# Performance work log

Hardware: AMD Instinct MI355X
Metric: run time of the kernel (lower is better)

## Reference

```python
import jax, jax.numpy as jnp
import numpy as np


def setup_inputs() -> dict:
    key = jax.random.key(0)
    k1, k2, k3 = jax.random.split(key, 3)
    preds = jax.random.normal(k1, (8, 3, 2048, 8), dtype=jnp.float32)
    gts = jax.random.normal(k2, (8, 3, 2048), dtype=jnp.float32)
    idx = jax.random.randint(k3, (64, 2), 0, 8, dtype=jnp.int64)
    return {"preds": preds, "gts": gts, "idx": idx}


def reference(preds, gts, idx):
    # preds: [bs, 3, N, seeds], gts: [bs, 3, N], idx: [num, 2] (batch, seed)
    num = idx.shape[0]
    # select (batch, seed) pairs -> [num, 3, N]
    p = jnp.transpose(preds, (0, 3, 1, 2))[idx[:, 0], idx[:, 1]]
    # gts expanded over seeds is constant in seed -> just index batch
    g = gts[idx[:, 0]]  # [num, 3, N]
    x = jnp.transpose(p, (0, 2, 1))  # [num, N, 3]
    y = jnp.transpose(g, (0, 2, 1))  # [num, N, 3]
    # P[b, i, j] = ||x_i||^2 + ||y_j||^2 - 2 x_i . y_j
    rx = jnp.sum(x * x, axis=-1)  # [num, N]
    ry = jnp.sum(y * y, axis=-1)  # [num, N]
    zz = jnp.einsum('bid,bjd->bij', x, y)  # [num, N, N]
    P = rx[:, :, None] + ry[:, None, :] - 2.0 * zz
    loss_1 = jnp.sum(jnp.min(P, axis=1))  # min over x for each y
    loss_2 = jnp.sum(jnp.min(P, axis=2))  # min over y for each x
    return (loss_1 + loss_2) / num
```

## Files before the change

kernel.cpp:

```cpp
#include <hip/hip_runtime.h>


#define NPTS 2048
#define NB 64
#define BLK 256

#define PREDS_A 49152
#define PREDS_C 16384
#define GTS_A 6144
#define GTS_C 2048

#define OFF_ROW   0
#define OFF_COL   524288
#define OFF_PART  1048576
#define OFF_YPK   1052672
#define WS_REQ    (OFF_YPK + NB * NPTS * 32)

using bf16x8  = __attribute__((ext_vector_type(8))) __bf16;
using short8v = __attribute__((ext_vector_type(8))) short;
using f32x16  = __attribute__((ext_vector_type(16))) float;

static __device__ __forceinline__ unsigned short f2bf(float f) {
    unsigned u = __float_as_uint(f);
    u = u + 0x7FFFu + ((u >> 16) & 1u);
    return (unsigned short)(u >> 16);
}
static __device__ __forceinline__ float bf2f(unsigned short h) {
    return __uint_as_float(((unsigned)h) << 16);
}
static __device__ __forceinline__ float min3f(float a, float b, float c) {
    return fminf(fminf(a, b), c);
}
static __device__ __forceinline__ float ctree(f32x16 a) {
    const float c0 = min3f(a[0], a[1], a[2]);
    const float c1 = min3f(a[3], a[4], a[5]);
    const float c2 = min3f(a[6], a[7], a[8]);
    const float c3 = min3f(a[9], a[10], a[11]);
    const float c4 = min3f(a[12], a[13], a[14]);
    const float d0 = min3f(c0, c1, a[15]);
    const float d1 = min3f(c2, c3, c4);
    return fminf(d0, d1);
}

__global__ __launch_bounds__(256) void cf_prep(
    const float* __restrict__ gts, const int* __restrict__ idx,
    unsigned* __restrict__ colbuf, unsigned short* __restrict__ ypk)
{
    const int blk = blockIdx.x, tid = threadIdx.x;
    if (blk < 512) {
        colbuf[blk * 256 + tid] = 0x7F800000u;
    } else {
        const unsigned short one = 0x3F80;
        const int p = (blk - 512) * 256 + tid;
        const int b = p >> 11, j = p & 2047;
        const int i0 = idx[2 * b];
        const float* gb = gts + i0 * GTS_A + j;
        const float y0 = gb[0], y1 = gb[GTS_C], y2 = gb[2 * GTS_C];
        const float ry = fmaf(y0, y0, fmaf(y1, y1, y2 * y2));
        const unsigned short h0 = f2bf(y0), h1 = f2bf(y1), h2 = f2bf(y2);
        const unsigned short l0 = f2bf(y0 - bf2f(h0));
        const unsigned short l1 = f2bf(y1 - bf2f(h1));
        const unsigned short l2 = f2bf(y2 - bf2f(h2));
        const unsigned short rh = f2bf(ry), rl = f2bf(ry - bf2f(rh));
        alignas(16) unsigned short t[16] =
            {h0, h1, h2, l0, l1, l2, h0, h1, h2, one, one, rh, rl, 0, 0, 0};
        uint4* dst = (uint4*)(ypk + (size_t)p * 16);
        dst[0] = *(const uint4*)&t[0];
        dst[1] = *(const uint4*)&t[8];
    }
}

__global__ __launch_bounds__(BLK, 4) void cf_mf4(
    const float* __restrict__ preds, const int* __restrict__ idx,
    const unsigned short* __restrict__ ypk,
    float* __restrict__ rowbuf, unsigned* __restrict__ colbuf)
{
    const int tid = threadIdx.x;
    const int strip = blockIdx.x & 15;
    const int b = blockIdx.x >> 4;

    __shared__ float scolw[4][NPTS];

    const int l = tid & 63, w = tid >> 6;
    const int lc = l & 31, lh = l >> 5;

    const int i0 = idx[2 * b], m1 = idx[2 * b + 1];
    {
    }
    const float* pb = preds + i0 * PREDS_A + m1 + (strip * 128 + w * 32 + lc) * 8;
    const float x0 = pb[0], x1 = pb[PREDS_C], x2 = pb[2 * PREDS_C];
    const float rx = fmaf(x0, x0, fmaf(x1, x1, x2 * x2));
    const float a0 = -2.f * x0, a1 = -2.f * x1, a2 = -2.f * x2;
    const unsigned short h0 = f2bf(a0), h1 = f2bf(a1), h2 = f2bf(a2);
    const unsigned short lo0 = f2bf(a0 - bf2f(h0));
    const unsigned short lo1 = f2bf(a1 - bf2f(h1));
    const unsigned short lo2 = f2bf(a2 - bf2f(h2));
    const unsigned short rh = f2bf(rx), rl = f2bf(rx - bf2f(rh));
    const unsigned short one = 0x3F80;
    short8v av;
    av[0] = (short)(lh ? lo2 : h0);
    av[1] = (short)(lh ? rh  : h1);
    av[2] = (short)(lh ? rl  : h2);
    av[3] = (short)(lh ? one : h0);
    av[4] = (short)(lh ? one : h1);
    av[5] = (short)(lh ? (unsigned short)0 : h2);
    av[6] = (short)(lh ? (unsigned short)0 : lo0);
    av[7] = (short)(lh ? (unsigned short)0 : lo1);
    const bf16x8 afrag = __builtin_bit_cast(bf16x8, av);

    float rm[16];
#pragma unroll
    for (int r = 0; r < 16; ++r) rm[r] = INFINITY;

    const f32x16 z = {0.f, 0.f, 0.f, 0.f, 0.f, 0.f, 0.f, 0.f,
                      0.f, 0.f, 0.f, 0.f, 0.f, 0.f, 0.f, 0.f};

    const short8v* yp = (const short8v*)ypk + (b * NPTS * 2 + lc * 2 + lh);

    bf16x8 curA = __builtin_bit_cast(bf16x8, yp[0]);
    bf16x8 curB = __builtin_bit_cast(bf16x8, yp[64]);

#pragma unroll 2
    for (int s = 0; s < 32; ++s) {
        const int nidx = (s < 31) ? (2 * s + 2) * 64 : 0;
        const bf16x8 nxtA = __builtin_bit_cast(bf16x8, yp[nidx]);
        const bf16x8 nxtB = __builtin_bit_cast(bf16x8, yp[nidx + 64]);

        __builtin_amdgcn_s_setprio(1);
        f32x16 accA = __builtin_amdgcn_mfma_f32_32x32x16_bf16(afrag, curA, z, 0, 0, 0);
        f32x16 accB = __builtin_amdgcn_mfma_f32_32x32x16_bf16(afrag, curB, z, 0, 0, 0);
        __builtin_amdgcn_s_setprio(0);

#pragma unroll
        for (int r = 0; r < 16; ++r) rm[r] = min3f(accA[r], accB[r], rm[r]);
        float cmA = ctree(accA);
        float cmB = ctree(accB);
        cmA = fminf(cmA, __shfl_xor(cmA, 32, 64));
        cmB = fminf(cmB, __shfl_xor(cmB, 32, 64));
        scolw[w][(2 * s) * 32 + lc] = cmA;
        scolw[w][(2 * s + 1) * 32 + lc] = cmB;

        curA = nxtA; curB = nxtB;
    }

#pragma unroll
    for (int r = 0; r < 16; ++r) {
        float v = rm[r];
        v = fminf(v, __shfl_xor(v, 1, 32));
        v = fminf(v, __shfl_xor(v, 2, 32));
        v = fminf(v, __shfl_xor(v, 4, 32));
        v = fminf(v, __shfl_xor(v, 8, 32));
        v = fminf(v, __shfl_xor(v, 16, 32));
        rm[r] = v;
    }
    if (lc == 0) {
        const int rbase = b * NPTS + strip * 128 + w * 32 + 4 * lh;
#pragma unroll
        for (int r = 0; r < 16; ++r)
            rowbuf[rbase + (r & 3) + 8 * (r >> 2)] = fmaxf(rm[r], 0.f);
    }

    __syncthreads();
    for (int k = tid; k < NPTS; k += BLK) {
        const float m = fminf(fminf(scolw[0][k], scolw[1][k]),
                              fminf(scolw[2][k], scolw[3][k]));
        atomicMin(&colbuf[b * NPTS + k], __float_as_uint(fmaxf(m, 0.f)));
    }
}

__global__ __launch_bounds__(256) void cf_red1(
    const float* __restrict__ rowbuf, const unsigned* __restrict__ colbuf,
    float* __restrict__ partial)
{
    __shared__ float sm[4];
    const int blk = blockIdx.x, tid = threadIdx.x;
    float s = 0.0f;
    if (blk < 64) {
        const float* rp = rowbuf + blk * 2048;
#pragma unroll
        for (int i = 0; i < 8; ++i) s += rp[tid + i * 256];
    } else {
        const unsigned* cp = colbuf + (blk - 64) * 2048;
#pragma unroll
        for (int i = 0; i < 8; ++i) s += __uint_as_float(cp[tid + i * 256]);
    }
#pragma unroll
    for (int off = 32; off > 0; off >>= 1)
        s += __shfl_down(s, off, 64);
    if ((tid & 63) == 0) sm[tid >> 6] = s;
    __syncthreads();
    if (tid == 0) partial[blk] = sm[0] + sm[1] + sm[2] + sm[3];
}

__global__ __launch_bounds__(256) void cf_red2(const float* __restrict__ partial,
                                               float* __restrict__ out) {
    __shared__ float sm[4];
    float s = (threadIdx.x < 128) ? partial[threadIdx.x] : 0.f;
#pragma unroll
    for (int off = 32; off > 0; off >>= 1)
        s += __shfl_down(s, off, 64);
    if ((threadIdx.x & 63) == 0) sm[threadIdx.x >> 6] = s;
    __syncthreads();
    if (threadIdx.x == 0)
        out[0] = (sm[0] + sm[1] + sm[2] + sm[3]) * (1.0f / 64.0f);
}

#define NMIN (2 * NB * NPTS)
#define FIT 128
#define FJT 128
#define PADI(j) ((j) + ((j) >> 4))

__global__ __launch_bounds__(256) void cf_init(unsigned* __restrict__ colbuf) {
    int i = blockIdx.x * 256 + threadIdx.x;
    colbuf[i] = 0x7F800000u;
}

__global__ __launch_bounds__(BLK, 4) void cf_tile_lds(
    const float* __restrict__ preds, const float* __restrict__ gts,
    const int* __restrict__ idx, unsigned* __restrict__ minbuf)
{
    const int tid = threadIdx.x;
    const int bid = blockIdx.x;
    const int it = bid & 15;
    const int b = bid >> 4;
    const int i0 = idx[2 * b];
    const int m1 = idx[2 * b + 1];
    const float* pbase = preds + i0 * PREDS_A + m1;
    const float* gbase = gts + i0 * GTS_A;

    __shared__ float4 sq[PADI(FIT - 1) + 2];
    __shared__ float4 sr[PADI(NPTS - 1) + 2];
    __shared__ float  scolw[4][FJT];

    if (tid < FIT) {
        const int i = it * FIT + tid;
        const float q0 = pbase[i * 8];
        const float q1 = pbase[i * 8 + PREDS_C];
        const float q2 = pbase[i * 8 + 2 * PREDS_C];
        const float rq = fmaf(q0, q0, fmaf(q1, q1, q2 * q2));
        sq[PADI(tid)] = make_float4(-2.f * q0, -2.f * q1, -2.f * q2, rq);
    }
#pragma unroll
    for (int k = 0; k < 8; ++k) {
        const int j = tid + BLK * k;
        const float r0 = gbase[j];
        const float r1 = gbase[j + GTS_C];
        const float r2 = gbase[j + 2 * GTS_C];
        const float rr = fmaf(r0, r0, fmaf(r1, r1, r2 * r2));
        sr[PADI(j)] = make_float4(r0, r1, r2, rr);
    }
    __syncthreads();

    const int ty = tid >> 4, tx = tid & 15;
    float nq0[8], nq1[8], nq2[8], rq[8], rmin[8];
#pragma unroll
    for (int u = 0; u < 8; ++u) {
        const float4 q = sq[PADI(ty * 8 + u)];
        nq0[u] = q.x; nq1[u] = q.y; nq2[u] = q.z; rq[u] = q.w;
        rmin[u] = INFINITY;
    }
    unsigned* rowbuf = minbuf;
    unsigned* colbuf = minbuf + NB * NPTS;

    for (int jt = 0; jt < NPTS / FJT; ++jt) {
        float4 r[8];
        const int rb = PADI(jt * FJT + tx * 8);
#pragma unroll
        for (int v = 0; v < 8; ++v) r[v] = sr[rb + v];
        float cmin[8];
#pragma unroll
        for (int v = 0; v < 8; ++v) cmin[v] = INFINITY;
#pragma unroll
        for (int v = 0; v < 8; v += 2) {
#pragma unroll
            for (int u = 0; u < 8; u += 2) {
                float s00 = fmaf(nq2[u], r[v].z, r[v].w);
                s00 = fmaf(nq1[u], r[v].y, s00);
                s00 = fmaf(nq0[u], r[v].x, s00);
                float s01 = fmaf(nq2[u], r[v + 1].z, r[v + 1].w);
                s01 = fmaf(nq1[u], r[v + 1].y, s01);
                s01 = fmaf(nq0[u], r[v + 1].x, s01);
                float s10 = fmaf(nq2[u + 1], r[v].z, r[v].w);
                s10 = fmaf(nq1[u + 1], r[v].y, s10);
                s10 = fmaf(nq0[u + 1], r[v].x, s10);
                float s11 = fmaf(nq2[u + 1], r[v + 1].z, r[v + 1].w);
                s11 = fmaf(nq1[u + 1], r[v + 1].y, s11);
                s11 = fmaf(nq0[u + 1], r[v + 1].x, s11);
                rmin[u]     = min3f(s00, s01, rmin[u]);
                rmin[u + 1] = min3f(s10, s11, rmin[u + 1]);
                const float d00 = s00 + rq[u];
                const float d10 = s10 + rq[u + 1];
                const float d01 = s01 + rq[u];
                const float d11 = s11 + rq[u + 1];
                cmin[v]     = min3f(d00, d10, cmin[v]);
                cmin[v + 1] = min3f(d01, d11, cmin[v + 1]);
            }
        }
#pragma unroll
        for (int v = 0; v < 8; ++v) {
            float c = cmin[v];
            c = fminf(c, __shfl_xor(c, 16, 64));
            c = fminf(c, __shfl_xor(c, 32, 64));
            cmin[v] = c;
        }
        if (((tid >> 4) & 3) == 0) {
            const int w = tid >> 6;
            *(float4*)&scolw[w][tx * 8]     = make_float4(cmin[0], cmin[1], cmin[2], cmin[3]);
            *(float4*)&scolw[w][tx * 8 + 4] = make_float4(cmin[4], cmin[5], cmin[6], cmin[7]);
        }
        __syncthreads();
        if (tid < FJT) {
            float m = fminf(min3f(scolw[0][tid], scolw[1][tid], scolw[2][tid]), scolw[3][tid]);
            m = fmaxf(m, 0.0f);
            atomicMin(&colbuf[b * NPTS + jt * FJT + tid], __float_as_uint(m));
        }
        __syncthreads();
    }
#pragma unroll
    for (int u = 0; u < 8; ++u) {
        float rm = rmin[u];
        rm = fminf(rm, __shfl_xor(rm, 1, 16));
        rm = fminf(rm, __shfl_xor(rm, 2, 16));
        rm = fminf(rm, __shfl_xor(rm, 4, 16));
        rm = fminf(rm, __shfl_xor(rm, 8, 16));
        rmin[u] = rm;
    }
    if (tx == 0) {
#pragma unroll
        for (int u = 0; u < 8; ++u) {
            const float d = fmaxf(rmin[u] + rq[u], 0.0f);
            rowbuf[b * NPTS + it * FIT + ty * 8 + u] = __float_as_uint(d);
        }
    }
}

__global__ __launch_bounds__(256) void cf_reduce1(const unsigned* __restrict__ minbuf,
                                                  float* __restrict__ partial) {
    __shared__ float sm[4];
    const int base = blockIdx.x * 1024;
    float s = 0.0f;
    for (int k = threadIdx.x; k < 1024; k += 256)
        s += __uint_as_float(minbuf[base + k]);
#pragma unroll
    for (int off = 32; off > 0; off >>= 1)
        s += __shfl_down(s, off, 64);
    if ((threadIdx.x & 63) == 0) sm[threadIdx.x >> 6] = s;
    __syncthreads();
    if (threadIdx.x == 0)
        partial[blockIdx.x] = sm[0] + sm[1] + sm[2] + sm[3];
}

__global__ __launch_bounds__(256) void cf_reduce2(const float* __restrict__ partial,
                                                  float* __restrict__ out) {
    __shared__ float sm[4];
    float s = (threadIdx.x < 128) ? partial[threadIdx.x] : 0.f;
#pragma unroll
    for (int off = 32; off > 0; off >>= 1)
        s += __shfl_down(s, off, 64);
    if ((threadIdx.x & 63) == 0) sm[threadIdx.x >> 6] = s;
    __syncthreads();
    if (threadIdx.x == 0)
        out[0] = (sm[0] + sm[1] + sm[2] + sm[3]) * (1.0f / 64.0f);
}

extern "C" void kernel_launch(void* const* d_in, const int* in_sizes, int n_in,
                              void* d_out, int out_size, void* d_ws, size_t ws_size,
                              hipStream_t stream) {
    const float* preds = (const float*)d_in[0];
    const float* gts   = (const float*)d_in[1];
    const int*   idx   = (const int*)d_in[2];
    float* out = (float*)d_out;

    if (ws_size >= (size_t)WS_REQ) {
        float*    rowbuf  = (float*)((char*)d_ws + OFF_ROW);
        unsigned* colbuf  = (unsigned*)((char*)d_ws + OFF_COL);
        float*    partial = (float*)((char*)d_ws + OFF_PART);
        unsigned short* ypk = (unsigned short*)((char*)d_ws + OFF_YPK);
        cf_prep<<<1024, 256, 0, stream>>>(gts, idx, colbuf, ypk);
        cf_mf4<<<NB * 16, BLK, 0, stream>>>(preds, idx, ypk, rowbuf, colbuf);
        cf_red1<<<128, 256, 0, stream>>>(rowbuf, colbuf, partial);
        cf_red2<<<1, 256, 0, stream>>>(partial, out);
    } else {
        unsigned* minbuf = (unsigned*)d_ws;
        unsigned* colbuf = minbuf + NB * NPTS;
        float* partial   = (float*)((char*)d_ws + NMIN * 4);
        cf_init<<<(NB * NPTS) / 256, 256, 0, stream>>>(colbuf);
        cf_tile_lds<<<NB * (NPTS / FIT), BLK, 0, stream>>>(preds, gts, idx, minbuf);
        cf_reduce1<<<NMIN / 1024, 256, 0, stream>>>(minbuf, partial);
        cf_reduce2<<<1, 256, 0, stream>>>(partial, out);
    }
}
```

Measured before the change: 37.75 us.

## Compute column minima via a second symmetric MFMA pass instead of atomics

```diff
diff --git a/kernel.cpp b/kernel.cpp
--- a/kernel.cpp
+++ b/kernel.cpp
@@ -10,11 +10,12 @@
 #define GTS_A 6144
 #define GTS_C 2048
 
-#define OFF_ROW   0
-#define OFF_COL   524288
+#define OFF_XMIN  0
+#define OFF_YMIN  524288
 #define OFF_PART  1048576
-#define OFF_YPK   1052672
-#define WS_REQ    (OFF_YPK + NB * NPTS * 32)
+#define OFF_XPK   1052672
+#define OFF_YPK   5246976
+#define WS_REQ    9441280
 
 using bf16x8  = __attribute__((ext_vector_type(8))) __bf16;
 using short8v = __attribute__((ext_vector_type(8))) short;
@@ -31,64 +32,67 @@
 static __device__ __forceinline__ float min3f(float a, float b, float c) {
     return fminf(fminf(a, b), c);
 }
-static __device__ __forceinline__ float ctree(f32x16 a) {
-    const float c0 = min3f(a[0], a[1], a[2]);
-    const float c1 = min3f(a[3], a[4], a[5]);
-    const float c2 = min3f(a[6], a[7], a[8]);
-    const float c3 = min3f(a[9], a[10], a[11]);
-    const float c4 = min3f(a[12], a[13], a[14]);
-    const float d0 = min3f(c0, c1, a[15]);
-    const float d1 = min3f(c2, c3, c4);
-    return fminf(d0, d1);
-}
-
-__global__ __launch_bounds__(256) void cf_prep(
-    const float* __restrict__ gts, const int* __restrict__ idx,
-    unsigned* __restrict__ colbuf, unsigned short* __restrict__ ypk)
+
+__global__ __launch_bounds__(256) void cf_prep3(
+    const float* __restrict__ preds, const float* __restrict__ gts,
+    const int* __restrict__ idx,
+    unsigned short* __restrict__ xpkB, unsigned short* __restrict__ ypkB)
 {
     const int blk = blockIdx.x, tid = threadIdx.x;
+    const unsigned short one = 0x3F80;
+    const int p = (blk & 511) * 256 + tid;
+    const int b = p >> 11, j = p & 2047;
+    const int i0 = idx[2 * b];
+    float v0, v1, v2;
+    unsigned short* dstbase;
     if (blk < 512) {
-        colbuf[blk * 256 + tid] = 0x7F800000u;
+        const int m1 = idx[2 * b + 1];
+        const float* pb = preds + i0 * PREDS_A + m1 + j * 8;
+        v0 = pb[0]; v1 = pb[PREDS_C]; v2 = pb[2 * PREDS_C];
+        dstbase = xpkB;
     } else {
-        const unsigned short one = 0x3F80;
-        const int p = (blk - 512) * 256 + tid;
-        const int b = p >> 11, j = p & 2047;
-        const int i0 = idx[2 * b];
         const float* gb = gts + i0 * GTS_A + j;
-        const float y0 = gb[0], y1 = gb[GTS_C], y2 = gb[2 * GTS_C];
-        const float ry = fmaf(y0, y0, fmaf(y1, y1, y2 * y2));
-        const unsigned short h0 = f2bf(y0), h1 = f2bf(y1), h2 = f2bf(y2);
-        const unsigned short l0 = f2bf(y0 - bf2f(h0));
-        const unsigned short l1 = f2bf(y1 - bf2f(h1));
-        const unsigned short l2 = f2bf(y2 - bf2f(h2));
-        const unsigned short rh = f2bf(ry), rl = f2bf(ry - bf2f(rh));
-        alignas(16) unsigned short t[16] =
-            {h0, h1, h2, l0, l1, l2, h0, h1, h2, one, one, rh, rl, 0, 0, 0};
-        uint4* dst = (uint4*)(ypk + (size_t)p * 16);
-        dst[0] = *(const uint4*)&t[0];
-        dst[1] = *(const uint4*)&t[8];
-    }
-}
-
-__global__ __launch_bounds__(BLK, 4) void cf_mf4(
-    const float* __restrict__ preds, const int* __restrict__ idx,
-    const unsigned short* __restrict__ ypk,
-    float* __restrict__ rowbuf, unsigned* __restrict__ colbuf)
+        v0 = gb[0]; v1 = gb[GTS_C]; v2 = gb[2 * GTS_C];
+        dstbase = ypkB;
+    }
+    const float rr = fmaf(v0, v0, fmaf(v1, v1, v2 * v2));
+    const unsigned short h0 = f2bf(v0), h1 = f2bf(v1), h2 = f2bf(v2);
+    const unsigned short l0 = f2bf(v0 - bf2f(h0));
+    const unsigned short l1 = f2bf(v1 - bf2f(h1));
+    const unsigned short l2 = f2bf(v2 - bf2f(h2));
+    const unsigned short rh = f2bf(rr), rl = f2bf(rr - bf2f(rh));
+    alignas(16) unsigned short t[16] =
+        {h0, h1, h2, l0, l1, l2, h0, h1, h2, one, one, rh, rl, 0, 0, 0};
+    uint4* dst = (uint4*)(dstbase + (size_t)p * 16);
+    dst[0] = *(const uint4*)&t[0];
+    dst[1] = *(const uint4*)&t[8];
+}
+
+__global__ __launch_bounds__(BLK, 4) void cf_mf5(
+    const float* __restrict__ preds, const float* __restrict__ gts,
+    const int* __restrict__ idx,
+    const unsigned short* __restrict__ xpkB, const unsigned short* __restrict__ ypkB,
+    float* __restrict__ xmin, float* __restrict__ ymin)
 {
     const int tid = threadIdx.x;
+    const int pass = blockIdx.x >> 10;
     const int strip = blockIdx.x & 15;
-    const int b = blockIdx.x >> 4;
-
-    __shared__ float scolw[4][NPTS];
+    const int b = (blockIdx.x >> 4) & 63;
 
     const int l = tid & 63, w = tid >> 6;
     const int lc = l & 31, lh = l >> 5;
 
-    const int i0 = idx[2 * b], m1 = idx[2 * b + 1];
-    {
-    }
-    const float* pb = preds + i0 * PREDS_A + m1 + (strip * 128 + w * 32 + lc) * 8;
-    const float x0 = pb[0], x1 = pb[PREDS_C], x2 = pb[2 * PREDS_C];
+    const int i0 = idx[2 * b];
+    const int row = strip * 128 + w * 32 + lc;
+    float x0, x1, x2;
+    if (pass == 0) {
+        const int m1 = idx[2 * b + 1];
+        const float* pb = preds + i0 * PREDS_A + m1 + row * 8;
+        x0 = pb[0]; x1 = pb[PREDS_C]; x2 = pb[2 * PREDS_C];
+    } else {
+        const float* gb = gts + i0 * GTS_A + row;
+        x0 = gb[0]; x1 = gb[GTS_C]; x2 = gb[2 * GTS_C];
+    }
     const float rx = fmaf(x0, x0, fmaf(x1, x1, x2 * x2));
     const float a0 = -2.f * x0, a1 = -2.f * x1, a2 = -2.f * x2;
     const unsigned short h0 = f2bf(a0), h1 = f2bf(a1), h2 = f2bf(a2);
@@ -115,7 +119,8 @@
     const f32x16 z = {0.f, 0.f, 0.f, 0.f, 0.f, 0.f, 0.f, 0.f,
                       0.f, 0.f, 0.f, 0.f, 0.f, 0.f, 0.f, 0.f};
 
-    const short8v* yp = (const short8v*)ypk + (b * NPTS * 2 + lc * 2 + lh);
+    const unsigned short* refpk = pass ? xpkB : ypkB;
+    const short8v* yp = (const short8v*)refpk + (b * NPTS * 2 + lc * 2 + lh);
 
     bf16x8 curA = __builtin_bit_cast(bf16x8, yp[0]);
     bf16x8 curB = __builtin_bit_cast(bf16x8, yp[64]);
@@ -133,12 +138,6 @@
 
 #pragma unroll
         for (int r = 0; r < 16; ++r) rm[r] = min3f(accA[r], accB[r], rm[r]);
-        float cmA = ctree(accA);
-        float cmB = ctree(accB);
-        cmA = fminf(cmA, __shfl_xor(cmA, 32, 64));
-        cmB = fminf(cmB, __shfl_xor(cmB, 32, 64));
-        scolw[w][(2 * s) * 32 + lc] = cmA;
-        scolw[w][(2 * s + 1) * 32 + lc] = cmB;
 
         curA = nxtA; curB = nxtB;
     }
@@ -154,36 +153,24 @@
         rm[r] = v;
     }
     if (lc == 0) {
+        float* outbuf = pass ? ymin : xmin;
         const int rbase = b * NPTS + strip * 128 + w * 32 + 4 * lh;
 #pragma unroll
         for (int r = 0; r < 16; ++r)
-            rowbuf[rbase + (r & 3) + 8 * (r >> 2)] = fmaxf(rm[r], 0.f);
-    }
-
-    __syncthreads();
-    for (int k = tid; k < NPTS; k += BLK) {
-        const float m = fminf(fminf(scolw[0][k], scolw[1][k]),
-                              fminf(scolw[2][k], scolw[3][k]));
-        atomicMin(&colbuf[b * NPTS + k], __float_as_uint(fmaxf(m, 0.f)));
+            outbuf[rbase + (r & 3) + 8 * (r >> 2)] = fmaxf(rm[r], 0.f);
     }
 }
 
 __global__ __launch_bounds__(256) void cf_red1(
-    const float* __restrict__ rowbuf, const unsigned* __restrict__ colbuf,
+    const float* __restrict__ xmin, const float* __restrict__ ymin,
     float* __restrict__ partial)
 {
     __shared__ float sm[4];
     const int blk = blockIdx.x, tid = threadIdx.x;
+    const float* rp = (blk < 64) ? (xmin + blk * 2048) : (ymin + (blk - 64) * 2048);
     float s = 0.0f;
-    if (blk < 64) {
-        const float* rp = rowbuf + blk * 2048;
-#pragma unroll
-        for (int i = 0; i < 8; ++i) s += rp[tid + i * 256];
-    } else {
-        const unsigned* cp = colbuf + (blk - 64) * 2048;
-#pragma unroll
-        for (int i = 0; i < 8; ++i) s += __uint_as_float(cp[tid + i * 256]);
-    }
+#pragma unroll
+    for (int i = 0; i < 8; ++i) s += rp[tid + i * 256];
 #pragma unroll
     for (int off = 32; off > 0; off >>= 1)
         s += __shfl_down(s, off, 64);
@@ -372,13 +359,14 @@
     float* out = (float*)d_out;
 
     if (ws_size >= (size_t)WS_REQ) {
-        float*    rowbuf  = (float*)((char*)d_ws + OFF_ROW);
-        unsigned* colbuf  = (unsigned*)((char*)d_ws + OFF_COL);
-        float*    partial = (float*)((char*)d_ws + OFF_PART);
-        unsigned short* ypk = (unsigned short*)((char*)d_ws + OFF_YPK);
-        cf_prep<<<1024, 256, 0, stream>>>(gts, idx, colbuf, ypk);
-        cf_mf4<<<NB * 16, BLK, 0, stream>>>(preds, idx, ypk, rowbuf, colbuf);
-        cf_red1<<<128, 256, 0, stream>>>(rowbuf, colbuf, partial);
+        float* xmin = (float*)((char*)d_ws + OFF_XMIN);
+        float* ymin = (float*)((char*)d_ws + OFF_YMIN);
+        float* partial = (float*)((char*)d_ws + OFF_PART);
+        unsigned short* xpkB = (unsigned short*)((char*)d_ws + OFF_XPK);
+        unsigned short* ypkB = (unsigned short*)((char*)d_ws + OFF_YPK);
+        cf_prep3<<<1024, 256, 0, stream>>>(preds, gts, idx, xpkB, ypkB);
+        cf_mf5<<<2 * NB * 16, BLK, 0, stream>>>(preds, gts, idx, xpkB, ypkB, xmin, ymin);
+        cf_red1<<<128, 256, 0, stream>>>(xmin, ymin, partial);
         cf_red2<<<1, 256, 0, stream>>>(partial, out);
     } else {
         unsigned* minbuf = (unsigned*)d_ws;
```

Result: slower. 41.31 us (+9.4%).
